# Optimization experiments

Hardware: AMD Instinct MI355X
Metric: run time of the kernel (lower is better)

Reference implementation:

```python
import jax, jax.numpy as jnp
import numpy as np

N = 100000
E = 1600000
IN_C, HID_C, OUT_C = 64, 64, 40

def setup_inputs() -> dict:
    key = jax.random.key(0)
    ks = jax.random.split(key, 12)
    x = jax.random.normal(ks[0], (N, IN_C), dtype=jnp.float32)
    edge_index = jax.random.randint(ks[1], (2, E), 0, N, dtype=jnp.int32)
    def glorot(k, fan_in, fan_out):
        lim = float(np.sqrt(6.0 / (fan_in + fan_out)))
        return jax.random.uniform(k, (fan_in, fan_out), jnp.float32, -lim, lim)
    return {
        "x": x,
        "edge_index": edge_index,
        "W0_0": glorot(ks[2], IN_C, HID_C), "W1_0": glorot(ks[3], IN_C, HID_C), "b_0": jnp.zeros((HID_C,), jnp.float32),
        "W0_1": glorot(ks[4], HID_C, HID_C), "W1_1": glorot(ks[5], HID_C, HID_C), "b_1": jnp.zeros((HID_C,), jnp.float32),
        "W0_2": glorot(ks[6], HID_C, OUT_C), "W1_2": glorot(ks[7], HID_C, OUT_C), "b_2": jnp.zeros((OUT_C,), jnp.float32),
    }

def _cheb_norm(edge_index, num_nodes, dtype):
    # PyG ChebConv.__norm__ with normalization=None, edge_weight=None -> ones.
    # L = D - A; lambda_max = 2 * max(L weights); scaled: 2L/lambda_max - I.
    src, dst = edge_index[0], edge_index[1]
    w = jnp.ones((edge_index.shape[1],), dtype)
    deg = jax.ops.segment_sum(w, src, num_segments=num_nodes)
    lam = 2.0 * jnp.maximum(jnp.max(deg), jnp.max(-w))
    scale = 2.0 / lam
    norm_edge = -w * scale            # off-diagonal entries
    norm_loop = deg * scale - 1.0     # diagonal entries (self-loop mask subtracts 1)
    return norm_edge, norm_loop

def _spmm(x, src, dst, norm_edge, norm_loop, num_nodes):
    # y[i] = sum_{e: src->i} norm_e * x[src_e] + norm_loop[i] * x[i]
    msg = norm_edge[:, None] * x[src]
    return jax.ops.segment_sum(msg, dst, num_segments=num_nodes) + norm_loop[:, None] * x

def reference(x, edge_index, W0_0, W1_0, b_0, W0_1, W1_1, b_1, W0_2, W1_2, b_2):
    num_nodes = x.shape[0]
    src, dst = edge_index[0], edge_index[1]
    norm_edge, norm_loop = _cheb_norm(edge_index, num_nodes, x.dtype)

    def cheb(h, W0, W1, b):
        # K=2: out = T0(L) h W0 + T1(L) h W1 + b, T0 = I, T1 = scaled L
        Tx1 = _spmm(h, src, dst, norm_edge, norm_loop, num_nodes)
        return h @ W0 + Tx1 @ W1 + b

    h = jax.nn.relu(cheb(x, W0_0, W1_0, b_0))   # dropout is identity in eval mode
    h = jax.nn.relu(cheb(h, W0_1, W1_1, b_1))
    h = cheb(h, W0_2, W1_2, b_2)
    return jax.nn.log_softmax(h, axis=-1)
```

## Files before the change

### kernel.cpp

```cpp
#include <hip/hip_runtime.h>
#include <math.h>

#define N_NODES 100000
#define N_EDGES 1600000
#define OUTC 40
#define PAIRS40 20

#define NC 32
#define CHUNK (N_EDGES / NC)

#define NPH 100032
#define RANGE_F 32768
#define NR_F 4
#define NPB 131072

#define FILLB (NC * NR_F)
#define NB32 (N_NODES / 32)
#define GEMB ((NB32 + 3) / 4)

#define SCAN_BLOCK 1024
#define SCAN_NBLK ((N_NODES + SCAN_BLOCK - 1) / SCAN_BLOCK)

typedef float vf2 __attribute__((ext_vector_type(2)));
typedef __fp16 f16x2 __attribute__((ext_vector_type(2)));

__device__ inline unsigned pack_bf16x2(float lo, float hi) {
    unsigned a = __float_as_uint(lo), b = __float_as_uint(hi);
    a = (a + 0x7fffu + ((a >> 16) & 1u)) >> 16;
    b = (b + 0x7fffu + ((b >> 16) & 1u)) & 0xffff0000u;
    return a | b;
}
__device__ inline float bf_lo(unsigned u) { return __uint_as_float(u << 16); }
__device__ inline float bf_hi(unsigned u) { return __uint_as_float(u & 0xffff0000u); }

__device__ inline unsigned pk16(float a, float b) {
    f16x2 h = __builtin_amdgcn_cvt_pkrtz(a, b);
    return __builtin_bit_cast(unsigned, h);
}
__device__ inline f16x2 uph(unsigned u) { return __builtin_bit_cast(f16x2, u); }

__device__ inline float fdot2(f16x2 a, f16x2 b, float c) {
#if __has_builtin(__builtin_amdgcn_fdot2)
    return __builtin_amdgcn_fdot2(a, b, c, false);
#else
    float d;
    asm volatile("v_dot2_f32_f16 %0, %1, %2, %3" : "=v"(d) : "v"(a), "v"(b), "v"(c));
    return d;
#endif
}

#define DOT2_KP4(hq, w0_, w1_, w2_, w3_, p)                                  \
    {                                                                        \
        f16x2 h0 = uph((hq).x), h1 = uph((hq).y), h2 = uph((hq).z), h3 = uph((hq).w); \
        a0x[p] = fdot2(h0, uph((w0_).x), a0x[p]);                            \
        a0y[p] = fdot2(h0, uph((w0_).y), a0y[p]);                            \
        a1x[p] = fdot2(h0, uph((w0_).z), a1x[p]);                            \
        a1y[p] = fdot2(h0, uph((w0_).w), a1y[p]);                            \
        a0x[p] = fdot2(h1, uph((w1_).x), a0x[p]);                            \
        a0y[p] = fdot2(h1, uph((w1_).y), a0y[p]);                            \
        a1x[p] = fdot2(h1, uph((w1_).z), a1x[p]);                            \
        a1y[p] = fdot2(h1, uph((w1_).w), a1y[p]);                            \
        a0x[p] = fdot2(h2, uph((w2_).x), a0x[p]);                            \
        a0y[p] = fdot2(h2, uph((w2_).y), a0y[p]);                            \
        a1x[p] = fdot2(h2, uph((w2_).z), a1x[p]);                            \
        a1y[p] = fdot2(h2, uph((w2_).w), a1y[p]);                            \
        a0x[p] = fdot2(h3, uph((w3_).x), a0x[p]);                            \
        a0y[p] = fdot2(h3, uph((w3_).y), a0y[p]);                            \
        a1x[p] = fdot2(h3, uph((w3_).z), a1x[p]);                            \
        a1y[p] = fdot2(h3, uph((w3_).w), a1y[p]);                            \
    }

__global__ __launch_bounds__(1024) void k_hist(const int* __restrict__ src,
                                               const int* __restrict__ dst,
                                               unsigned char* __restrict__ Hs,
                                               unsigned char* __restrict__ Hd) {
    __shared__ unsigned h32[NPH / 4];
    int c = blockIdx.x;
    const int* a = blockIdx.y ? dst : src;
    unsigned char* H = blockIdx.y ? Hd : Hs;
    for (int k = threadIdx.x; k < NPH / 4; k += 1024) h32[k] = 0;
    __syncthreads();
    const int4* a4 = (const int4*)(a + c * CHUNK);
    for (int k = threadIdx.x; k < CHUNK / 4; k += 1024) {
        int4 v = a4[k];
        atomicAdd(&h32[v.x >> 2], 1u << ((v.x & 3) * 8));
        atomicAdd(&h32[v.y >> 2], 1u << ((v.y & 3) * 8));
        atomicAdd(&h32[v.z >> 2], 1u << ((v.z & 3) * 8));
        atomicAdd(&h32[v.w >> 2], 1u << ((v.w & 3) * 8));
    }
    __syncthreads();
    unsigned* Hw = (unsigned*)(H + (size_t)c * NPH);
    for (int k = threadIdx.x; k < NPH / 4; k += 1024) Hw[k] = h32[k];
}

__global__ __launch_bounds__(SCAN_BLOCK) void k_scan1(const unsigned char* __restrict__ Hs,
                                                      const unsigned char* __restrict__ Hd,
                                                      int* __restrict__ rowptr,
                                                      int* __restrict__ blocksum,
                                                      int* __restrict__ deg_src,
                                                      int* __restrict__ maxdeg) {
    __shared__ int buf[2][SCAN_BLOCK];
    int t = threadIdx.x;
    int i = blockIdx.x * SCAN_BLOCK + t;
    int vs = 0, vd = 0;
    if (i < N_NODES) {
        #pragma unroll
        for (int c = 0; c < NC; c++) { vs += Hs[(size_t)c * NPH + i]; vd += Hd[(size_t)c * NPH + i]; }
        deg_src[i] = vs;
    }
    int m = vs;
    for (int off = 32; off; off >>= 1) m = max(m, __shfl_down(m, off));
    if ((t & 63) == 0) atomicMax(maxdeg, m);
    int pd = (vd + 7) & ~7;
    int cur = 0;
    buf[0][t] = pd;
    __syncthreads();
    for (int off = 1; off < SCAN_BLOCK; off <<= 1) {
        int nv = buf[cur][t];
        if (t >= off) nv += buf[cur][t - off];
        buf[1 - cur][t] = nv;
        cur = 1 - cur;
        __syncthreads();
    }
    int incl = buf[cur][t];
    if (i < N_NODES) rowptr[i + 1] = incl;
    if (t == SCAN_BLOCK - 1) blocksum[blockIdx.x] = incl;
}

__global__ __launch_bounds__(SCAN_BLOCK) void k_finalize(const int* __restrict__ blocksum,
                                                         int* __restrict__ rowptr,
                                                         const unsigned char* __restrict__ Hd,
                                                         int* __restrict__ Bd,
                                                         int* __restrict__ csr_src) {
    __shared__ int soff;
    int t = threadIdx.x, blk = blockIdx.x;
    if (t == 0) {
        int r = 0;
        for (int j = 0; j < blk; j++) r += blocksum[j];
        soff = r;
        if (blk == 0) rowptr[0] = 0;
    }
    __syncthreads();
    int i = blk * SCAN_BLOCK + t;
    if (i >= N_NODES) return;
    int tmp[NC];
    int s = 0;
    #pragma unroll
    for (int c = 0; c < NC; c++) { tmp[c] = Hd[(size_t)c * NPH + i]; s += tmp[c]; }
    int rf = rowptr[i + 1] + soff;
    rowptr[i + 1] = rf;
    int pd = (s + 7) & ~7;
    int run = rf - pd;
    #pragma unroll
    for (int c = 0; c < NC; c++) { Bd[(size_t)c * NPB + i] = run; run += tmp[c]; }
    for (int k = run; k < rf; k++) csr_src[k] = N_NODES;
}

__global__ __launch_bounds__(1024) void k_fill_gemm(const int* __restrict__ src,
                                                    const int* __restrict__ dst,
                                                    const int* __restrict__ basepos,
                                                    int* __restrict__ csr_src,
                                                    const float* __restrict__ hf,
                                                    const float* __restrict__ W0,
                                                    const float* __restrict__ W1,
                                                    const float* __restrict__ b,
                                                    const int* __restrict__ deg_src,
                                                    const int* __restrict__ maxdeg,
                                                    unsigned* __restrict__ G0b,
                                                    unsigned short* __restrict__ G1f8) {
    __shared__ union {
        int pos[RANGE_F];
        struct { uint4 swu[32 * 32]; unsigned shu[4 * 1024]; } g;
    } sm;
    int t = threadIdx.x;
    if (blockIdx.x < FILLB) {
        int c = blockIdx.x & 31, r = blockIdx.x >> 5;
        int r0 = r * RANGE_F;
        const int4* bp4 = (const int4*)(basepos + (size_t)c * NPB + r0);
        for (int k = t; k < RANGE_F / 4; k += 1024) ((int4*)sm.pos)[k] = bp4[k];
        __syncthreads();
        const int4* d4 = (const int4*)(dst + c * CHUNK);
        const int4* s4 = (const int4*)(src + c * CHUNK);
        for (int k = t; k < CHUNK / 4; k += 1024) {
            int4 dv = d4[k];
            int4 sv = s4[k];
            unsigned q0 = (unsigned)(dv.x - r0);
            unsigned q1 = (unsigned)(dv.y - r0);
            unsigned q2 = (unsigned)(dv.z - r0);
            unsigned q3 = (unsigned)(dv.w - r0);
            if (q0 < RANGE_F) csr_src[atomicAdd(&sm.pos[q0], 1)] = sv.x;
            if (q1 < RANGE_F) csr_src[atomicAdd(&sm.pos[q1], 1)] = sv.y;
            if (q2 < RANGE_F) csr_src[atomicAdd(&sm.pos[q2], 1)] = sv.z;
            if (q3 < RANGE_F) csr_src[atomicAdd(&sm.pos[q3], 1)] = sv.w;
        }
        return;
    }
    int gb = blockIdx.x - FILLB;
    int sub = t >> 8, tt = t & 255;
    int nb = gb * 4 + sub;
    bool ok = nb < NB32;
    const float2* W02 = (const float2*)W0;
    const float2* W12 = (const float2*)W1;
    {
        int kp = t >> 5, c2 = t & 31;
        float2 a  = W02[(kp * 2) * 32 + c2];
        float2 bb = W02[(kp * 2 + 1) * 32 + c2];
        float2 cc = W12[(kp * 2) * 32 + c2];
        float2 dd = W12[(kp * 2 + 1) * 32 + c2];
        sm.g.swu[t] = make_uint4(pk16(a.x, bb.x), pk16(a.y, bb.y), pk16(cc.x, dd.x), pk16(cc.y, dd.y));
    }
    if (ok) {
        const float4* h4 = (const float4*)(hf + (size_t)(nb * 32) * 64);
        float4 f0 = h4[tt * 2], f1 = h4[tt * 2 + 1];
        ((uint4*)(sm.g.shu + sub * 1024))[tt] =
            make_uint4(pk16(f0.x, f0.y), pk16(f0.z, f0.w), pk16(f1.x, f1.y), pk16(f1.z, f1.w));
    }
    if (blockIdx.x == FILLB && t < 16) ((unsigned*)G1f8)[N_NODES * 16 + t] = 0;
    __syncthreads();
    if (!ok) return;
    int c2 = tt & 31, rg = tt >> 5;
    int i0 = nb * 32;
    const unsigned* shu = sm.g.shu + sub * 1024;
    float scale = 1.0f / (float)(*maxdeg);
    float2 b2 = ((const float2*)b)[c2];
    float a0x[4], a0y[4], a1x[4], a1y[4];
    #pragma unroll
    for (int p = 0; p < 4; p++) { a0x[p] = b2.x; a0y[p] = b2.y; a1x[p] = 0.f; a1y[p] = 0.f; }
    #pragma unroll
    for (int kp4 = 0; kp4 < 32; kp4 += 4) {
        uint4 w0 = sm.g.swu[(kp4 + 0) * 32 + c2];
        uint4 w1 = sm.g.swu[(kp4 + 1) * 32 + c2];
        uint4 w2 = sm.g.swu[(kp4 + 2) * 32 + c2];
        uint4 w3 = sm.g.swu[(kp4 + 3) * 32 + c2];
        #pragma unroll
        for (int p = 0; p < 4; p++) {
            uint4 hq = ((const uint4*)(shu + (rg + 8 * p) * 32))[kp4 >> 2];
            DOT2_KP4(hq, w0, w1, w2, w3, p);
        }
    }
    #pragma unroll
    for (int p = 0; p < 4; p++) {
        int row = i0 + rg + 8 * p;
        float nl = (float)deg_src[row] * scale - 1.0f;
        G0b[row * 32 + c2] = pack_bf16x2(a0x[p] + nl * a1x[p], a0y[p] + nl * a1y[p]);
        int pk = __builtin_amdgcn_cvt_pk_fp8_f32(a1x[p], a1y[p], 0, false);
        G1f8[row * 32 + c2] = (unsigned short)(pk & 0xffff);
    }
}

__global__ __launch_bounds__(256, 6) void k_fs64_g64(const unsigned* __restrict__ G0b_in,
                                                     const unsigned char* __restrict__ g1_in,
                                                     const int* __restrict__ rowptr,
                                                     const int* __restrict__ csr_src,
                                                     const int* __restrict__ deg_src,
                                                     const int* __restrict__ maxdeg,
                                                     const float* __restrict__ W0,
                                                     const float* __restrict__ W1,
                                                     const float* __restrict__ b,
                                                     unsigned* __restrict__ G0b_out,
                                                     unsigned short* __restrict__ G1f8_out) {
    __shared__ uint4 swu[32 * 32];
    __shared__ unsigned shu[32 * 32];
    int t = threadIdx.x;
    const float2* W02 = (const float2*)W0;
    const float2* W12 = (const float2*)W1;
    for (int cell = t; cell < 1024; cell += 256) {
        int kp = cell >> 5, c2 = cell & 31;
        float2 a  = W02[(kp * 2) * 32 + c2];
        float2 bb = W02[(kp * 2 + 1) * 32 + c2];
        float2 cc = W12[(kp * 2) * 32 + c2];
        float2 dd = W12[(kp * 2 + 1) * 32 + c2];
        swu[cell] = make_uint4(pk16(a.x, bb.x), pk16(a.y, bb.y), pk16(cc.x, dd.x), pk16(cc.y, dd.y));
    }
    int waveId = t >> 6, lane = t & 63;
    int ch = lane & 7;
    int local = waveId * 8 + (lane >> 3);
    int node = blockIdx.x * 32 + local;
    float scale = 1.0f / (float)(*maxdeg);
    int e0 = rowptr[node], e1 = rowptr[node + 1];
    int octbase = lane & 56;
    vf2 acc[4];
    acc[0] = 0.f; acc[1] = 0.f; acc[2] = 0.f; acc[3] = 0.f;
    uint2 u[8], n[8];
    int idxC = 0;
    int e = e0;
    if (e < e1) {
        int idxA = csr_src[e + ch];
        int idxB = 0;
        if (e + 8 < e1)  idxB = csr_src[e + 8 + ch];
        if (e + 16 < e1) idxC = csr_src[e + 16 + ch];
        #pragma unroll
        for (int j = 0; j < 8; j++) {
            int s = __shfl(idxA, octbase | j);
            u[j] = ((const uint2*)(g1_in + (size_t)s * 64))[ch];
        }
        if (e + 8 < e1) {
            #pragma unroll
            for (int j = 0; j < 8; j++) {
                int s = __shfl(idxB, octbase | j);
                n[j] = ((const uint2*)(g1_in + (size_t)s * 64))[ch];
            }
        }
    }
    while (e < e1) {
        int en = e + 8;
        int idxD = 0;
        if (en + 16 < e1) idxD = csr_src[en + 16 + ch];
        uint2 m[8];
        if (en + 8 < e1) {
            #pragma unroll
            for (int j = 0; j < 8; j++) {
                int s = __shfl(idxC, octbase | j);
                m[j] = ((const uint2*)(g1_in + (size_t)s * 64))[ch];
            }
        }
        #pragma unroll
        for (int j = 0; j < 8; j++) {
            acc[0] += __builtin_amdgcn_cvt_pk_f32_fp8((int)u[j].x, false);
            acc[1] += __builtin_amdgcn_cvt_pk_f32_fp8((int)u[j].x, true);
            acc[2] += __builtin_amdgcn_cvt_pk_f32_fp8((int)u[j].y, false);
            acc[3] += __builtin_amdgcn_cvt_pk_f32_fp8((int)u[j].y, true);
        }
        #pragma unroll
        for (int j = 0; j < 8; j++) { u[j] = n[j]; n[j] = m[j]; }
        idxC = idxD;
        e = en;
    }
    uint4 g = ((const uint4*)(G0b_in + (size_t)node * 32))[ch];
    float v0 = fmaxf(bf_lo(g.x) - scale * acc[0].x, 0.f);
    float v1 = fmaxf(bf_hi(g.x) - scale * acc[0].y, 0.f);
    float v2 = fmaxf(bf_lo(g.y) - scale * acc[1].x, 0.f);
    float v3 = fmaxf(bf_hi(g.y) - scale * acc[1].y, 0.f);
    float v4 = fmaxf(bf_lo(g.z) - scale * acc[2].x, 0.f);
    float v5 = fmaxf(bf_hi(g.z) - scale * acc[2].y, 0.f);
    float v6 = fmaxf(bf_lo(g.w) - scale * acc[3].x, 0.f);
    float v7 = fmaxf(bf_hi(g.w) - scale * acc[3].y, 0.f);
    ((uint4*)shu)[local * 8 + ch] = make_uint4(pk16(v0, v1), pk16(v2, v3), pk16(v4, v5), pk16(v6, v7));
    if (blockIdx.x == 0 && t < 16) ((unsigned*)G1f8_out)[N_NODES * 16 + t] = 0;
    __syncthreads();
    int c2 = t & 31, rg = t >> 5;
    int i0 = blockIdx.x * 32;
    float2 b2 = ((const float2*)b)[c2];
    float a0x[4], a0y[4], a1x[4], a1y[4];
    #pragma unroll
    for (int p = 0; p < 4; p++) { a0x[p] = b2.x; a0y[p] = b2.y; a1x[p] = 0.f; a1y[p] = 0.f; }
    #pragma unroll
    for (int kp4 = 0; kp4 < 32; kp4 += 4) {
        uint4 w0 = swu[(kp4 + 0) * 32 + c2];
        uint4 w1 = swu[(kp4 + 1) * 32 + c2];
        uint4 w2 = swu[(kp4 + 2) * 32 + c2];
        uint4 w3 = swu[(kp4 + 3) * 32 + c2];
        #pragma unroll
        for (int p = 0; p < 4; p++) {
            uint4 hq = ((const uint4*)(shu + (rg + 8 * p) * 32))[kp4 >> 2];
            DOT2_KP4(hq, w0, w1, w2, w3, p);
        }
    }
    #pragma unroll
    for (int p = 0; p < 4; p++) {
        int row = i0 + rg + 8 * p;
        float nl = (float)deg_src[row] * scale - 1.0f;
        G0b_out[row * 32 + c2] = pack_bf16x2(a0x[p] + nl * a1x[p], a0y[p] + nl * a1y[p]);
        int pk = __builtin_amdgcn_cvt_pk_fp8_f32(a1x[p], a1y[p], 0, false);
        G1f8_out[row * 32 + c2] = (unsigned short)(pk & 0xffff);
    }
}

__global__ __launch_bounds__(256, 6) void k_fs64_g40(const unsigned* __restrict__ G0b_in,
                                                     const unsigned char* __restrict__ g1_in,
                                                     const int* __restrict__ rowptr,
                                                     const int* __restrict__ csr_src,
                                                     const int* __restrict__ deg_src,
                                                     const int* __restrict__ maxdeg,
                                                     const float* __restrict__ W0,
                                                     const float* __restrict__ W1,
                                                     const float* __restrict__ b,
                                                     unsigned* __restrict__ G0b_out,
                                                     unsigned short* __restrict__ G1f8_out) {
    __shared__ uint4 swu[32 * PAIRS40];
    __shared__ unsigned shu[32 * 32];
    int t = threadIdx.x;
    const float2* W02 = (const float2*)W0;
    const float2* W12 = (const float2*)W1;
    for (int cell = t; cell < 32 * PAIRS40; cell += 256) {
        int kp = cell / PAIRS40, c2 = cell % PAIRS40;
        float2 a  = W02[(kp * 2) * PAIRS40 + c2];
        float2 bb = W02[(kp * 2 + 1) * PAIRS40 + c2];
        float2 cc = W12[(kp * 2) * PAIRS40 + c2];
        float2 dd = W12[(kp * 2 + 1) * PAIRS40 + c2];
        swu[cell] = make_uint4(pk16(a.x, bb.x), pk16(a.y, bb.y), pk16(cc.x, dd.x), pk16(cc.y, dd.y));
    }
    int waveId = t >> 6, lane = t & 63;
    int ch = lane & 7;
    int local = waveId * 8 + (lane >> 3);
    int node = blockIdx.x * 32 + local;
    float scale = 1.0f / (float)(*maxdeg);
    int e0 = rowptr[node], e1 = rowptr[node + 1];
    int octbase = lane & 56;
    vf2 acc[4];
    acc[0] = 0.f; acc[1] = 0.f; acc[2] = 0.f; acc[3] = 0.f;
    uint2 u[8], n[8];
    int idxC = 0;
    int e = e0;
    if (e < e1) {
        int idxA = csr_src[e + ch];
        int idxB = 0;
        if (e + 8 < e1)  idxB = csr_src[e + 8 + ch];
        if (e + 16 < e1) idxC = csr_src[e + 16 + ch];
        #pragma unroll
        for (int j = 0; j < 8; j++) {
            int s = __shfl(idxA, octbase | j);
            u[j] = ((const uint2*)(g1_in + (size_t)s * 64))[ch];
        }
        if (e + 8 < e1) {
            #pragma unroll
            for (int j = 0; j < 8; j++) {
                int s = __shfl(idxB, octbase | j);
                n[j] = ((const uint2*)(g1_in + (size_t)s * 64))[ch];
            }
        }
    }
    while (e < e1) {
        int en = e + 8;
        int idxD = 0;
        if (en + 16 < e1) idxD = csr_src[en + 16 + ch];
        uint2 m[8];
        if (en + 8 < e1) {
            #pragma unroll
            for (int j = 0; j < 8; j++) {
                int s = __shfl(idxC, octbase | j);
                m[j] = ((const uint2*)(g1_in + (size_t)s * 64))[ch];
            }
        }
        #pragma unroll
        for (int j = 0; j < 8; j++) {
            acc[0] += __builtin_amdgcn_cvt_pk_f32_fp8((int)u[j].x, false);
            acc[1] += __builtin_amdgcn_cvt_pk_f32_fp8((int)u[j].x, true);
            acc[2] += __builtin_amdgcn_cvt_pk_f32_fp8((int)u[j].y, false);
            acc[3] += __builtin_amdgcn_cvt_pk_f32_fp8((int)u[j].y, true);
        }
        #pragma unroll
        for (int j = 0; j < 8; j++) { u[j] = n[j]; n[j] = m[j]; }
        idxC = idxD;
        e = en;
    }
    uint4 g = ((const uint4*)(G0b_in + (size_t)node * 32))[ch];
    float v0 = fmaxf(bf_lo(g.x) - scale * acc[0].x, 0.f);
    float v1 = fmaxf(bf_hi(g.x) - scale * acc[0].y, 0.f);
    float v2 = fmaxf(bf_lo(g.y) - scale * acc[1].x, 0.f);
    float v3 = fmaxf(bf_hi(g.y) - scale * acc[1].y, 0.f);
    float v4 = fmaxf(bf_lo(g.z) - scale * acc[2].x, 0.f);
    float v5 = fmaxf(bf_hi(g.z) - scale * acc[2].y, 0.f);
    float v6 = fmaxf(bf_lo(g.w) - scale * acc[3].x, 0.f);
    float v7 = fmaxf(bf_hi(g.w) - scale * acc[3].y, 0.f);
    ((uint4*)shu)[local * 8 + ch] = make_uint4(pk16(v0, v1), pk16(v2, v3), pk16(v4, v5), pk16(v6, v7));
    if (blockIdx.x == 0 && t < 16) ((unsigned*)G1f8_out)[N_NODES * 16 + t] = 0;
    __syncthreads();
    int c2 = t & 31, rg = t >> 5;
    if (c2 >= PAIRS40) return;
    int i0 = blockIdx.x * 32;
    float2 b2 = ((const float2*)b)[c2];
    float a0x[4], a0y[4], a1x[4], a1y[4];
    #pragma unroll
    for (int p = 0; p < 4; p++) { a0x[p] = b2.x; a0y[p] = b2.y; a1x[p] = 0.f; a1y[p] = 0.f; }
    #pragma unroll
    for (int kp4 = 0; kp4 < 32; kp4 += 4) {
        uint4 w0 = swu[(kp4 + 0) * PAIRS40 + c2];
        uint4 w1 = swu[(kp4 + 1) * PAIRS40 + c2];
        uint4 w2 = swu[(kp4 + 2) * PAIRS40 + c2];
        uint4 w3 = swu[(kp4 + 3) * PAIRS40 + c2];
        #pragma unroll
        for (int p = 0; p < 4; p++) {
            uint4 hq = ((const uint4*)(shu + (rg + 8 * p) * 32))[kp4 >> 2];
            DOT2_KP4(hq, w0, w1, w2, w3, p);
        }
    }
    #pragma unroll
    for (int p = 0; p < 4; p++) {
        int row = i0 + rg + 8 * p;
        float nl = (float)deg_src[row] * scale - 1.0f;
        G0b_out[row * PAIRS40 + c2] = pack_bf16x2(a0x[p] + nl * a1x[p], a0y[p] + nl * a1y[p]);
        int pk = __builtin_amdgcn_cvt_pk_fp8_f32(a1x[p], a1y[p], 0, false);
        G1f8_out[row * 32 + c2] = (unsigned short)(pk & 0xffff);
    }
}

__global__ __launch_bounds__(256, 6) void k_spmm40(const unsigned* __restrict__ G0b,
                                                   const unsigned char* __restrict__ g1,
                                                   const int* __restrict__ rowptr,
                                                   const int* __restrict__ csr_src,
                                                   const int* __restrict__ maxdeg,
                                                   float* __restrict__ out) {
    int t = threadIdx.x;
    int waveId = t >> 6, lane = t & 63;
    int ch = lane & 7;
    bool act = ch < 5;
    int node = blockIdx.x * 32 + waveId * 8 + (lane >> 3);
    float scale = 1.0f / (float)(*maxdeg);
    int e0 = rowptr[node], e1 = rowptr[node + 1];
    int octbase = lane & 56;
    vf2 acc[4];
    acc[0] = 0.f; acc[1] = 0.f; acc[2] = 0.f; acc[3] = 0.f;
    uint2 u[8], n[8];
    int idxC = 0;
    int e = e0;
    if (e < e1) {
        int idxA = csr_src[e + ch];
        int idxB = 0;
        if (e + 8 < e1)  idxB = csr_src[e + 8 + ch];
        if (e + 16 < e1) idxC = csr_src[e + 16 + ch];
        #pragma unroll
        for (int j = 0; j < 8; j++) {
            int s = __shfl(idxA, octbase | j);
            if (act) u[j] = ((const uint2*)(g1 + (size_t)s * 64))[ch];
        }
        if (e + 8 < e1) {
            #pragma unroll
            for (int j = 0; j < 8; j++) {
                int s = __shfl(idxB, octbase | j);
                if (act) n[j] = ((const uint2*)(g1 + (size_t)s * 64))[ch];
            }
        }
    }
    while (e < e1) {
        int en = e + 8;
        int idxD = 0;
        if (en + 16 < e1) idxD = csr_src[en + 16 + ch];
        uint2 m[8];
        if (en + 8 < e1) {
            #pragma unroll
            for (int j = 0; j < 8; j++) {
                int s = __shfl(idxC, octbase | j);
                if (act) m[j] = ((const uint2*)(g1 + (size_t)s * 64))[ch];
            }
        }
        if (act) {
            #pragma unroll
            for (int j = 0; j < 8; j++) {
                acc[0] += __builtin_amdgcn_cvt_pk_f32_fp8((int)u[j].x, false);
                acc[1] += __builtin_amdgcn_cvt_pk_f32_fp8((int)u[j].x, true);
                acc[2] += __builtin_amdgcn_cvt_pk_f32_fp8((int)u[j].y, false);
                acc[3] += __builtin_amdgcn_cvt_pk_f32_fp8((int)u[j].y, true);
            }
        }
        #pragma unroll
        for (int j = 0; j < 8; j++) { u[j] = n[j]; n[j] = m[j]; }
        idxC = idxD;
        e = en;
    }
    float v[8];
    float m = -INFINITY;
    if (act) {
        uint4 g = ((const uint4*)(G0b + (size_t)node * PAIRS40))[ch];
        v[0] = bf_lo(g.x) - scale * acc[0].x;
        v[1] = bf_hi(g.x) - scale * acc[0].y;
        v[2] = bf_lo(g.y) - scale * acc[1].x;
        v[3] = bf_hi(g.y) - scale * acc[1].y;
        v[4] = bf_lo(g.z) - scale * acc[2].x;
        v[5] = bf_hi(g.z) - scale * acc[2].y;
        v[6] = bf_lo(g.w) - scale * acc[3].x;
        v[7] = bf_hi(g.w) - scale * acc[3].y;
        #pragma unroll
        for (int q = 0; q < 8; q++) m = fmaxf(m, v[q]);
    }
    m = fmaxf(m, __shfl_xor(m, 1));
    m = fmaxf(m, __shfl_xor(m, 2));
    m = fmaxf(m, __shfl_xor(m, 4));
    float s = 0.f;
    if (act) {
        #pragma unroll
        for (int q = 0; q < 8; q++) s += __expf(v[q] - m);
    }
    s += __shfl_xor(s, 1);
    s += __shfl_xor(s, 2);
    s += __shfl_xor(s, 4);
    float ls = __logf(s);
    if (act) {
        float4 oA, oB;
        oA.x = v[0] - m - ls; oA.y = v[1] - m - ls; oA.z = v[2] - m - ls; oA.w = v[3] - m - ls;
        oB.x = v[4] - m - ls; oB.y = v[5] - m - ls; oB.z = v[6] - m - ls; oB.w = v[7] - m - ls;
        float4* o4 = (float4*)(out + (size_t)node * 40);
        o4[ch * 2] = oA;
        o4[ch * 2 + 1] = oB;
    }
}


extern "C" void kernel_launch(void* const* d_in, const int* in_sizes, int n_in,
                              void* d_out, int out_size, void* d_ws, size_t ws_size,
                              hipStream_t stream) {
    const float* x   = (const float*)d_in[0];
    const int* ei    = (const int*)d_in[1];
    const int* src   = ei;
    const int* dst   = ei + N_EDGES;
    const float* W0_0 = (const float*)d_in[2];
    const float* W1_0 = (const float*)d_in[3];
    const float* b_0  = (const float*)d_in[4];
    const float* W0_1 = (const float*)d_in[5];
    const float* W1_1 = (const float*)d_in[6];
    const float* b_1  = (const float*)d_in[7];
    const float* W0_2 = (const float*)d_in[8];
    const float* W1_2 = (const float*)d_in[9];
    const float* b_2  = (const float*)d_in[10];
    float* outp = (float*)d_out;

    int* ip = (int*)d_ws;
    int* deg_src  = ip;
    int* rowptr   = ip + 100000;
    int* blocksum = ip + 200064;
    int* maxdeg   = ip + 200192;
    int* csr_src  = ip + 200256;
    unsigned char* Hs = (unsigned char*)(ip + 2700256);
    unsigned char* Hd = (unsigned char*)(ip + 4797408);
    int* Bd       = ip + 6894560;
    unsigned* GA0 = (unsigned*)(ip + 11088864);
    unsigned short* GA1 = (unsigned short*)(ip + 14288864);
    unsigned* GB0 = (unsigned*)(ip + 15888928);
    unsigned short* GB1 = (unsigned short*)(ip + 19088928);

    (void)hipMemsetAsync(maxdeg, 0, sizeof(int), stream);

    k_hist<<<dim3(NC, 2), 1024, 0, stream>>>(src, dst, Hs, Hd);
    k_scan1<<<SCAN_NBLK, SCAN_BLOCK, 0, stream>>>(Hs, Hd, rowptr, blocksum, deg_src, maxdeg);
    k_finalize<<<SCAN_NBLK, SCAN_BLOCK, 0, stream>>>(blocksum, rowptr, Hd, Bd, csr_src);

    k_fill_gemm<<<FILLB + GEMB, 1024, 0, stream>>>(src, dst, Bd, csr_src,
                                                   x, W0_0, W1_0, b_0, deg_src, maxdeg, GA0, GA1);

    const int GS = N_NODES / 32;

    k_fs64_g64<<<GS, 256, 0, stream>>>(GA0, (const unsigned char*)GA1, rowptr, csr_src,
                                       deg_src, maxdeg, W0_1, W1_1, b_1, GB0, GB1);
    k_fs64_g40<<<GS, 256, 0, stream>>>(GB0, (const unsigned char*)GB1, rowptr, csr_src,
                                       deg_src, maxdeg, W0_2, W1_2, b_2, GA0, GA1);
    k_spmm40<<<GS, 256, 0, stream>>>(GA0, (const unsigned char*)GA1, rowptr, csr_src, maxdeg, outp);
}
```

Baseline: 272.7 us.

## Fuse scan and finalize into single-pass decoupled chained scan, drop memset

Merges the two scan kernels into one pass that chains block offsets through global flags with acquire/release atomics. Each block waits for its predecessor's running total. The destination histogram is read once and kept in registers, where before it was read again in the finalize kernel. The memset of maxdeg moves into the histogram kernel, which also resets the flags. This saves one kernel launch, one memset and a second pass over Hd. The cost is a serial spin-wait chain across roughly 98 blocks, which relies on earlier blocks making forward progress.

```diff
diff --git a/kernel.cpp b/kernel.cpp
--- a/kernel.cpp
+++ b/kernel.cpp
@@ -73,9 +73,15 @@
 __global__ __launch_bounds__(1024) void k_hist(const int* __restrict__ src,
                                                const int* __restrict__ dst,
                                                unsigned char* __restrict__ Hs,
-                                               unsigned char* __restrict__ Hd) {
+                                               unsigned char* __restrict__ Hd,
+                                               int* __restrict__ maxdeg,
+                                               int* __restrict__ gflag) {
     __shared__ unsigned h32[NPH / 4];
     int c = blockIdx.x;
+    if (c == 0 && blockIdx.y == 0) {
+        if (threadIdx.x == 0) *maxdeg = 0;
+        if (threadIdx.x < SCAN_NBLK) gflag[threadIdx.x] = -1;
+    }
     const int* a = blockIdx.y ? dst : src;
     unsigned char* H = blockIdx.y ? Hd : Hs;
     for (int k = threadIdx.x; k < NPH / 4; k += 1024) h32[k] = 0;
@@ -93,19 +99,27 @@
     for (int k = threadIdx.x; k < NPH / 4; k += 1024) Hw[k] = h32[k];
 }
 
-__global__ __launch_bounds__(SCAN_BLOCK) void k_scan1(const unsigned char* __restrict__ Hs,
-                                                      const unsigned char* __restrict__ Hd,
-                                                      int* __restrict__ rowptr,
-                                                      int* __restrict__ blocksum,
-                                                      int* __restrict__ deg_src,
-                                                      int* __restrict__ maxdeg) {
+__global__ __launch_bounds__(SCAN_BLOCK) void k_scan(const unsigned char* __restrict__ Hs,
+                                                     const unsigned char* __restrict__ Hd,
+                                                     int* __restrict__ rowptr,
+                                                     int* __restrict__ deg_src,
+                                                     int* __restrict__ maxdeg,
+                                                     int* __restrict__ gflag,
+                                                     int* __restrict__ Bd,
+                                                     int* __restrict__ csr_src) {
     __shared__ int buf[2][SCAN_BLOCK];
-    int t = threadIdx.x;
-    int i = blockIdx.x * SCAN_BLOCK + t;
+    __shared__ int s_soff, s_tot;
+    int t = threadIdx.x, blk = blockIdx.x;
+    int i = blk * SCAN_BLOCK + t;
+    int tmp[NC];
     int vs = 0, vd = 0;
     if (i < N_NODES) {
         #pragma unroll
-        for (int c = 0; c < NC; c++) { vs += Hs[(size_t)c * NPH + i]; vd += Hd[(size_t)c * NPH + i]; }
+        for (int c = 0; c < NC; c++) {
+            int h = Hd[(size_t)c * NPH + i];
+            tmp[c] = h; vd += h;
+            vs += Hs[(size_t)c * NPH + i];
+        }
         deg_src[i] = vs;
     }
     int m = vs;
@@ -123,37 +137,28 @@
         __syncthreads();
     }
     int incl = buf[cur][t];
-    if (i < N_NODES) rowptr[i + 1] = incl;
-    if (t == SCAN_BLOCK - 1) blocksum[blockIdx.x] = incl;
-}
-
-__global__ __launch_bounds__(SCAN_BLOCK) void k_finalize(const int* __restrict__ blocksum,
-                                                         int* __restrict__ rowptr,
-                                                         const unsigned char* __restrict__ Hd,
-                                                         int* __restrict__ Bd,
-                                                         int* __restrict__ csr_src) {
-    __shared__ int soff;
-    int t = threadIdx.x, blk = blockIdx.x;
+    if (t == SCAN_BLOCK - 1) s_tot = incl;
+    __syncthreads();
     if (t == 0) {
-        int r = 0;
-        for (int j = 0; j < blk; j++) r += blocksum[j];
-        soff = r;
-        if (blk == 0) rowptr[0] = 0;
-    }
-    __syncthreads();
-    int i = blk * SCAN_BLOCK + t;
+        int soff = 0;
+        if (blk > 0) {
+            while ((soff = __hip_atomic_load(&gflag[blk - 1], __ATOMIC_ACQUIRE,
+                                             __HIP_MEMORY_SCOPE_AGENT)) < 0) {}
+        } else {
+            rowptr[0] = 0;
+        }
+        __hip_atomic_store(&gflag[blk], soff + s_tot, __ATOMIC_RELEASE,
+                           __HIP_MEMORY_SCOPE_AGENT);
+        s_soff = soff;
+    }
+    __syncthreads();
     if (i >= N_NODES) return;
-    int tmp[NC];
-    int s = 0;
-    #pragma unroll
-    for (int c = 0; c < NC; c++) { tmp[c] = Hd[(size_t)c * NPH + i]; s += tmp[c]; }
-    int rf = rowptr[i + 1] + soff;
+    int rf = incl + s_soff;
     rowptr[i + 1] = rf;
-    int pd = (s + 7) & ~7;
     int run = rf - pd;
     #pragma unroll
     for (int c = 0; c < NC; c++) { Bd[(size_t)c * NPB + i] = run; run += tmp[c]; }
-    for (int k = run; k < rf; k++) csr_src[k] = N_NODES;
+    for (int k = run + 0; k < rf; k++) csr_src[k] = N_NODES;
 }
 
 __global__ __launch_bounds__(1024) void k_fill_gemm(const int* __restrict__ src,
@@ -607,7 +612,7 @@
     int* ip = (int*)d_ws;
     int* deg_src  = ip;
     int* rowptr   = ip + 100000;
-    int* blocksum = ip + 200064;
+    int* gflag    = ip + 200064;
     int* maxdeg   = ip + 200192;
     int* csr_src  = ip + 200256;
     unsigned char* Hs = (unsigned char*)(ip + 2700256);
@@ -618,11 +623,8 @@
     unsigned* GB0 = (unsigned*)(ip + 15888928);
     unsigned short* GB1 = (unsigned short*)(ip + 19088928);
 
-    (void)hipMemsetAsync(maxdeg, 0, sizeof(int), stream);
-
-    k_hist<<<dim3(NC, 2), 1024, 0, stream>>>(src, dst, Hs, Hd);
-    k_scan1<<<SCAN_NBLK, SCAN_BLOCK, 0, stream>>>(Hs, Hd, rowptr, blocksum, deg_src, maxdeg);
-    k_finalize<<<SCAN_NBLK, SCAN_BLOCK, 0, stream>>>(blocksum, rowptr, Hd, Bd, csr_src);
+    k_hist<<<dim3(NC, 2), 1024, 0, stream>>>(src, dst, Hs, Hd, maxdeg, gflag);
+    k_scan<<<SCAN_NBLK, SCAN_BLOCK, 0, stream>>>(Hs, Hd, rowptr, deg_src, maxdeg, gflag, Bd, csr_src);
 
     k_fill_gemm<<<FILLB + GEMB, 1024, 0, stream>>>(src, dst, Bd, csr_src,
                                                    x, W0_0, W1_0, b_0, deg_src, maxdeg, GA0, GA1);
```

Measured after the change: 419.2 us. 53.7% more time.
